# Performance work log

Hardware: AMD Instinct MI355X
Metric: run time of the kernel (lower is better)

The kernel has to match this reference:

```python
import jax, jax.numpy as jnp
import numpy as np

SG_SLOPE = 20.0  # fast_sigmoid surrogate slope
THRESHOLD = 1.0

@jax.custom_vjp
def spike_fn(v):
    # Heaviside spike with fast-sigmoid surrogate gradient
    return (v > 0).astype(v.dtype)

def _spike_fwd(v):
    return spike_fn(v), v

def _spike_bwd(v, g):
    return (g / (SG_SLOPE * jnp.abs(v) + 1.0) ** 2,)

spike_fn.defvjp(_spike_fwd, _spike_bwd)

def setup_inputs() -> dict:
    key = jax.random.key(0)
    T, IN, H, HEADS, O = 8192, 192, 1024, 5, 2
    dt = 0.004
    sp = float(np.log1p(np.exp(0.5413)))  # softplus(param) ~= 1.0
    tau_syn_h, tau_mem_h = 0.01 * sp, 0.02 * sp
    tau_syn_r = np.array([0.01, 0.02, 0.05, 0.1, 0.2]) * sp
    tau_mem_r = np.array([0.02, 0.05, 0.1, 0.2, 0.5]) * sp
    k1, k2, k3, k4 = jax.random.split(key, 4)
    x = jax.random.normal(k1, (T, IN), jnp.float32)
    W_in = jax.random.normal(k2, (H, IN), jnp.float32) / np.sqrt(IN)
    V = jax.random.normal(k3, (H, H), jnp.float32) / np.sqrt(H)
    b_rec = jnp.zeros((H,), jnp.float32)
    W_out = jax.random.normal(k4, (HEADS, O, H), jnp.float32) / np.sqrt(H)
    return {
        "x": x, "W_in": W_in, "V": V, "b_rec": b_rec, "W_out": W_out,
        "alpha_h": jnp.float32(np.exp(-dt / tau_syn_h)),
        "beta_h": jnp.float32(np.exp(-dt / tau_mem_h)),
        "alpha_r": jnp.asarray(np.exp(-dt / tau_syn_r), jnp.float32),
        "beta_r": jnp.asarray(np.exp(-dt / tau_mem_r), jnp.float32),
    }

def reference(x, W_in, V, b_rec, W_out, alpha_h, beta_h, alpha_r, beta_r):
    H = W_in.shape[0]
    HEADS, O, _ = W_out.shape
    dt_f32 = x.dtype

    def step(carry, x_t):
        inp_prev, spk, syn_h, mem_h, syn_r, mem_r = carry
        # hidden RSynaptic (note: fc_hidden consumes the PREVIOUS input, one-step delay)
        cur = W_in @ inp_prev + V @ spk + b_rec
        syn_h_new = alpha_h * syn_h + cur
        reset = jax.lax.stop_gradient(spk)  # zero-reset uses previous spike, detached
        mem_h_new = (beta_h * mem_h + syn_h_new) * (1.0 - reset)
        spk_new = spike_fn(mem_h_new - THRESHOLD)
        # readout heads consume the PREVIOUS hidden spike (pre-update)
        r_in = jnp.einsum("hoc,c->ho", W_out, spk)  # [HEADS, 2]
        syn_r_new = alpha_r[:, None] * syn_r + r_in
        mem_r_new = beta_r[:, None] * mem_r + syn_r_new  # reset_mechanism='none'
        out = mem_r_new.mean(axis=0)  # average over readout heads
        return (x_t, spk_new, syn_h_new, mem_h_new, syn_r_new, mem_r_new), out

    init = (
        jnp.zeros_like(x[0]),
        jnp.zeros((H,), dt_f32),
        jnp.zeros((H,), dt_f32),
        jnp.zeros((H,), dt_f32),
        jnp.zeros((HEADS, O), dt_f32),
        jnp.zeros((HEADS, O), dt_f32),
    )
    _, preds = jax.lax.scan(step, init, x)
    return preds  # [T, 2]
```

## Files before the change

kernel.cpp:

```cpp
#include <hip/hip_runtime.h>
#include <hip/hip_bf16.h>


constexpr int T_STEPS = 8192;
constexpr int IN_DIM  = 192;
constexpr int H_DIM   = 1024;
constexpr int NBLK    = 32;
constexpr int RING    = 4;

__global__ void k_clear(unsigned int* __restrict__ p, int n) {
    int i = blockIdx.x * blockDim.x + threadIdx.x;
    if (i < n) p[i] = 0u;
}

__global__ __launch_bounds__(576, 1) void k_phase1(
    const float* __restrict__ x,
    const float* __restrict__ W_in,
    const float* __restrict__ V,
    const float* __restrict__ b_rec,
    const float* __restrict__ alpha_h_p,
    const float* __restrict__ beta_h_p,
    unsigned long long* __restrict__ mbox,
    uint2* __restrict__ raster)
{
    const int tid   = threadIdx.x;
    const int blk   = blockIdx.x;
    const int w     = tid >> 6;
    const int l     = tid & 63;
    const bool syncw = (w == 8);
    const int r_local = l >> 4;
    const int cg      = l & 15;
    const int row   = (blk << 5) + (w << 2) + r_local;

    __shared__ unsigned int       bits_lds[RING][NBLK];
    __shared__ unsigned long long combine[2];
    __shared__ unsigned long long rdyPack;

    for (int i = tid; i < RING * NBLK; i += 576)
        ((unsigned int*)bits_lds)[i] = 0u;
    if (tid == 0) { combine[0] = 0ull; combine[1] = 0ull; rdyPack = 0ull; }

    unsigned int* rp = (unsigned int*)&rdyPack;

    float4 vfrag[16];
    float  wfrag[12];
    float  b_r = 0.f;
    if (!syncw) {
        const float4* vp = (const float4*)(V + (size_t)row * H_DIM + cg * 64);
        #pragma unroll
        for (int i = 0; i < 16; ++i) vfrag[i] = vp[i];
        const float* wp = W_in + row * IN_DIM + cg * 12;
        #pragma unroll
        for (int i = 0; i < 12; ++i) wfrag[i] = wp[i];
        b_r = b_rec[row];
    }
    const float ah = alpha_h_p[0];
    const float bh = beta_h_p[0];

    __syncthreads();

    float u0 = 1.02f, u1 = 1.03f, u2 = 1.05f, u3 = 1.07f;
    const float bc = 1.0000001f, bd = 1e-30f;

    if (syncw) {
        const bool act = (l < NBLK) && (l != blk);
        for (int t = 0; t < T_STEPS - 1; ++t) {
            const unsigned int want = (unsigned int)(t + 1);
            const unsigned long long* p =
                &mbox[(size_t)(((t & (RING - 1)) * NBLK + blk) * NBLK) + (l & 31)];
            unsigned long long vv = act
                ? __hip_atomic_load(p, __ATOMIC_RELAXED, __HIP_MEMORY_SCOPE_AGENT)
                : (((unsigned long long)want << 16) | ((unsigned long long)want << 48));
            bool ok = (((vv >> 16) & 0xffffull) == want) && ((vv >> 48) == want);
            while (__any(!ok)) {
                if (!ok)
                    vv = __hip_atomic_load(p, __ATOMIC_RELAXED,
                                           __HIP_MEMORY_SCOPE_AGENT);
                #pragma unroll
                for (int i = 0; i < 8; ++i) {
                    u0 = fmaf(u0, bc, bd); u1 = fmaf(u1, bc, bd);
                    u2 = fmaf(u2, bc, bd); u3 = fmaf(u3, bc, bd);
                }
                ok = (((vv >> 16) & 0xffffull) == want) && ((vv >> 48) == want);
            }
            if (act)
                bits_lds[t & (RING - 1)][l] =
                    (unsigned int)(vv & 0xffffull)
                    | ((unsigned int)((vv >> 32) & 0xffffull) << 16);
            asm volatile("s_waitcnt lgkmcnt(0)" ::: "memory");
            __builtin_amdgcn_sched_barrier(0);
            if (l == 0)
                __hip_atomic_store(&rp[0], (unsigned int)(t + 1),
                                   __ATOMIC_RELAXED, __HIP_MEMORY_SCOPE_WORKGROUP);
        }
    } else {
        const float* xptr = x + cg * 12;
        float xr[12];
        #pragma unroll
        for (int i = 0; i < 12; ++i) xr[i] = 0.0f;
        float syn = 0.f, mem = 0.f, prev = 0.f;

        for (int t = 0; t < T_STEPS; ++t) {
            const float4* xp4 = (const float4*)xptr;
            float4 f0 = xp4[0], f1 = xp4[1], f2 = xp4[2];

            unsigned long long rv = __hip_atomic_load(&rdyPack, __ATOMIC_ACQUIRE,
                                        __HIP_MEMORY_SCOPE_WORKGROUP);
            while ((unsigned int)rv < (unsigned int)t ||
                   (unsigned int)(rv >> 32) < (unsigned int)t) {
                #pragma unroll
                for (int i = 0; i < 4; ++i) {
                    u0 = fmaf(u0, bc, bd); u1 = fmaf(u1, bc, bd);
                    u2 = fmaf(u2, bc, bd); u3 = fmaf(u3, bc, bd);
                }
                rv = __hip_atomic_load(&rdyPack, __ATOMIC_ACQUIRE,
                                       __HIP_MEMORY_SCOPE_WORKGROUP);
            }

            const int slot = (t + RING - 1) & (RING - 1);
            unsigned int b0 = bits_lds[slot][2 * cg];
            unsigned int b1 = bits_lds[slot][2 * cg + 1];

            float a0 = 0.f, a1 = 0.f;
            #pragma unroll
            for (int i = 0; i < 8; ++i) {
                a0 = fmaf((float)((b0 >> (4 * i + 0)) & 1u), vfrag[i].x, a0);
                a0 = fmaf((float)((b0 >> (4 * i + 1)) & 1u), vfrag[i].y, a0);
                a0 = fmaf((float)((b0 >> (4 * i + 2)) & 1u), vfrag[i].z, a0);
                a0 = fmaf((float)((b0 >> (4 * i + 3)) & 1u), vfrag[i].w, a0);
                a1 = fmaf((float)((b1 >> (4 * i + 0)) & 1u), vfrag[8 + i].x, a1);
                a1 = fmaf((float)((b1 >> (4 * i + 1)) & 1u), vfrag[8 + i].y, a1);
                a1 = fmaf((float)((b1 >> (4 * i + 2)) & 1u), vfrag[8 + i].z, a1);
                a1 = fmaf((float)((b1 >> (4 * i + 3)) & 1u), vfrag[8 + i].w, a1);
            }
            #pragma unroll
            for (int i = 0; i < 12; ++i) a0 = fmaf(wfrag[i], xr[i], a0);
            float acc = a0 + a1;

            #pragma unroll
            for (int m = 1; m < 16; m <<= 1) acc += __shfl_xor(acc, m, 64);

            float cur = acc + b_r;
            syn = fmaf(ah, syn, cur);
            mem = fmaf(bh, mem, syn) * (1.0f - prev);
            float spk = (mem > 1.0f) ? 1.0f : 0.0f;
            prev = spk;

            unsigned long long bal = __ballot(spk > 0.5f);
            unsigned int isLast = 0u, bitsAll = 0u;
            if (l == 0) {
                unsigned int nib = (unsigned int)(bal & 1ull)
                                 | ((unsigned int)((bal >> 16) & 1ull) << 1)
                                 | ((unsigned int)((bal >> 32) & 1ull) << 2)
                                 | ((unsigned int)((bal >> 48) & 1ull) << 3);
                unsigned long long add =
                    (1ull << 32) | ((unsigned long long)nib << (4 * w));
                unsigned long long old = __hip_atomic_fetch_add(&combine[t & 1],
                        add, __ATOMIC_RELAXED, __HIP_MEMORY_SCOPE_WORKGROUP);
                unsigned long long nv = old + add;
                if ((nv >> 32) == 8ull) { isLast = 1u; bitsAll = (unsigned int)nv; }
            }
            isLast = __shfl(isLast, 0, 64);
            if (isLast) {
                unsigned int bits = __shfl(bitsAll, 0, 64);
                unsigned int want = (unsigned int)(t + 1);
                unsigned int w0t = (want << 16) | (bits & 0xffffu);
                unsigned int w1t = (want << 16) | (bits >> 16);
                unsigned long long pack =
                    (unsigned long long)w0t | ((unsigned long long)w1t << 32);
                if (l < NBLK && l != blk) {
                    __hip_atomic_store(
                        &mbox[(size_t)(((t & (RING - 1)) * NBLK + l) * NBLK) + blk],
                        pack, __ATOMIC_RELAXED, __HIP_MEMORY_SCOPE_AGENT);
                }
                if (l == 0) {
                    bits_lds[t & (RING - 1)][blk] = bits;
                    combine[t & 1] = 0ull;
                    asm volatile("s_waitcnt lgkmcnt(0)" ::: "memory");
                    __builtin_amdgcn_sched_barrier(0);
                    __hip_atomic_store(&rp[1], (unsigned int)(t + 1),
                                       __ATOMIC_RELAXED,
                                       __HIP_MEMORY_SCOPE_WORKGROUP);
                    raster[(size_t)t * NBLK + blk] = make_uint2(w0t, w1t);
                }
            }

            #pragma unroll
            for (int i = 0; i < 4; ++i) {
                xr[i]     = (&f0.x)[i];
                xr[4 + i] = (&f1.x)[i];
                xr[8 + i] = (&f2.x)[i];
            }
            xptr += IN_DIM;
        }
    }
    asm volatile("" :: "v"(u0), "v"(u1), "v"(u2), "v"(u3));
}

__global__ __launch_bounds__(256, 1) void k_readout_mm(
    const uint2* __restrict__ raster,
    const float* __restrict__ W_out,
    float* __restrict__ R)
{
    __shared__ float wlds[10 * 1033];
    for (int i = threadIdx.x; i < 10 * 1024; i += 256) {
        int r = i >> 10, c = i & 1023;
        wlds[r * 1033 + c] = W_out[i];
    }
    __syncthreads();

    int tid = threadIdx.x;
    if (tid >= 250) return;
    int tl = tid / 10, rowr = tid - tl * 10;
    int t = blockIdx.x * 25 + tl;
    if (t >= T_STEPS) return;

    float acc = 0.f;
    if (t > 0) {
        const uint2* wp = raster + (size_t)(t - 1) * NBLK;
        const float* wr = &wlds[rowr * 1033];
        for (int ww = 0; ww < NBLK; ++ww) {
            uint2 v = wp[ww];
            unsigned int bits = (v.x & 0xffffu) | ((v.y & 0xffffu) << 16);
            const float* wb = wr + ww * 32;
            #pragma unroll
            for (int j = 0; j < 32; ++j)
                acc = fmaf((float)((bits >> j) & 1u), wb[j], acc);
        }
    }
    R[t * 10 + rowr] = acc;
}

__global__ void k_scan(const float* __restrict__ R,
                       const float* __restrict__ alpha_r,
                       const float* __restrict__ beta_r,
                       float* __restrict__ memr_all)
{
    int lane = threadIdx.x;
    bool act = lane < 10;
    float a = act ? alpha_r[lane >> 1] : 0.f;
    float b = act ? beta_r[lane >> 1] : 0.f;
    float syn = 0.f, mem = 0.f;
    constexpr int PF = 8;
    float buf[PF];
    #pragma unroll
    for (int i = 0; i < PF; ++i) buf[i] = act ? R[i * 10 + lane] : 0.f;

    for (int tb = 0; tb < T_STEPS; tb += PF) {
        #pragma unroll
        for (int i = 0; i < PF; ++i) {
            int t = tb + i;
            syn = fmaf(a, syn, buf[i]);
            mem = fmaf(b, mem, syn);
            if (act) memr_all[t * 10 + lane] = mem;
            int tn = t + PF;
            buf[i] = (act && tn < T_STEPS) ? R[tn * 10 + lane] : 0.f;
        }
    }
}

__global__ void k_mean(const float* __restrict__ memr_all, float* __restrict__ out) {
    int g = blockIdx.x * blockDim.x + threadIdx.x;
    if (g >= T_STEPS * 2) return;
    int t = g >> 1, o = g & 1;
    const float* m = memr_all + t * 10 + o;
    out[g] = 0.2f * (m[0] + m[2] + m[4] + m[6] + m[8]);
}

extern "C" void kernel_launch(void* const* d_in, const int* in_sizes, int n_in,
                              void* d_out, int out_size, void* d_ws, size_t ws_size,
                              hipStream_t stream) {
    (void)in_sizes; (void)n_in; (void)out_size; (void)ws_size;
    const float* x       = (const float*)d_in[0];
    const float* W_in    = (const float*)d_in[1];
    const float* V       = (const float*)d_in[2];
    const float* b_rec   = (const float*)d_in[3];
    const float* W_out   = (const float*)d_in[4];
    const float* alpha_h = (const float*)d_in[5];
    const float* beta_h  = (const float*)d_in[6];
    const float* alpha_r = (const float*)d_in[7];
    const float* beta_r  = (const float*)d_in[8];
    float* out = (float*)d_out;

    char* wsb = (char*)d_ws;
    unsigned long long* mbox = (unsigned long long*)wsb;
    uint2* raster  = (uint2*)(wsb + RING * NBLK * NBLK * 8);
    float* Rbuf    = (float*)(wsb + RING * NBLK * NBLK * 8
                              + (size_t)T_STEPS * NBLK * 8);
    float* memr_all = Rbuf + (size_t)T_STEPS * 10;

    int nclr = RING * NBLK * NBLK * 2;
    k_clear<<<(nclr + 255) / 256, 256, 0, stream>>>((unsigned int*)mbox, nclr);
    k_phase1<<<NBLK, 576, 0, stream>>>(x, W_in, V, b_rec, alpha_h, beta_h,
                                       mbox, raster);
    k_readout_mm<<<(T_STEPS + 24) / 25, 256, 0, stream>>>(raster, W_out, Rbuf);
    k_scan<<<1, 64, 0, stream>>>(Rbuf, alpha_r, beta_r, memr_all);
    k_mean<<<(T_STEPS * 2 + 255) / 256, 256, 0, stream>>>(memr_all, out);
}
```

Measured before the change: 17.64 ms.

## Halve persistent workgroup count to 16 with 64 rows per block

Repartitions the recurrent step across 16 workgroups instead of 32, so each block owns 64 hidden rows and each lane holds twice as much of V in registers. The goal is fewer cross-block mailbox exchanges and pollers per timestep, cutting the global synchronisation latency that dominates the serial 8192-step loop. The intra-block spike combine is reworked around a 64-bit bit mask plus a separate counter, and the raster format becomes 64 bits per block. In exchange each lane does twice the FMA work and uses many more registers, and x is now loaded directly each step instead of being prefetched a step ahead.

Result: slower. 42.27 ms (+139.6%).

```diff
diff --git a/kernel.cpp b/kernel.cpp
--- a/kernel.cpp
+++ b/kernel.cpp
@@ -5,7 +5,7 @@
 constexpr int T_STEPS = 8192;
 constexpr int IN_DIM  = 192;
 constexpr int H_DIM   = 1024;
-constexpr int NBLK    = 32;
+constexpr int NBLK    = 16;
 constexpr int RING    = 4;
 
 __global__ void k_clear(unsigned int* __restrict__ p, int n) {
@@ -21,37 +21,44 @@
     const float* __restrict__ alpha_h_p,
     const float* __restrict__ beta_h_p,
     unsigned long long* __restrict__ mbox,
-    uint2* __restrict__ raster)
+    unsigned long long* __restrict__ raster)
 {
     const int tid   = threadIdx.x;
     const int blk   = blockIdx.x;
     const int w     = tid >> 6;
     const int l     = tid & 63;
     const bool syncw = (w == 8);
-    const int r_local = l >> 4;
-    const int cg      = l & 15;
-    const int row   = (blk << 5) + (w << 2) + r_local;
-
-    __shared__ unsigned int       bits_lds[RING][NBLK];
-    __shared__ unsigned long long combine[2];
+    const int r_local = l >> 3;
+    const int cg      = l & 7;
+    const int row   = (blk << 6) + (w << 3) + r_local;
+
+    __shared__ __align__(16) unsigned int bits_lds[RING][2 * NBLK];
+    __shared__ unsigned long long cbits[2];
+    __shared__ unsigned int       ccnt[2];
     __shared__ unsigned long long rdyPack;
 
-    for (int i = tid; i < RING * NBLK; i += 576)
+    for (int i = tid; i < RING * 2 * NBLK; i += 576)
         ((unsigned int*)bits_lds)[i] = 0u;
-    if (tid == 0) { combine[0] = 0ull; combine[1] = 0ull; rdyPack = 0ull; }
-
+    if (tid == 0) {
+        cbits[0] = 0ull; cbits[1] = 0ull;
+        ccnt[0] = 0u; ccnt[1] = 0u; rdyPack = 0ull;
+    }
     unsigned int* rp = (unsigned int*)&rdyPack;
 
-    float4 vfrag[16];
-    float  wfrag[12];
+    float4 vfrag[32];
+    float  wfrag[24];
     float  b_r = 0.f;
     if (!syncw) {
-        const float4* vp = (const float4*)(V + (size_t)row * H_DIM + cg * 64);
+        const float4* vp = (const float4*)(V + (size_t)row * H_DIM + cg * 128);
         #pragma unroll
-        for (int i = 0; i < 16; ++i) vfrag[i] = vp[i];
-        const float* wp = W_in + row * IN_DIM + cg * 12;
+        for (int i = 0; i < 32; ++i) vfrag[i] = vp[i];
+        const float4* wp = (const float4*)(W_in + row * IN_DIM + cg * 24);
         #pragma unroll
-        for (int i = 0; i < 12; ++i) wfrag[i] = wp[i];
+        for (int i = 0; i < 6; ++i) {
+            float4 v4 = wp[i];
+            wfrag[4 * i]     = v4.x; wfrag[4 * i + 1] = v4.y;
+            wfrag[4 * i + 2] = v4.z; wfrag[4 * i + 3] = v4.w;
+        }
         b_r = b_rec[row];
     }
     const float ah = alpha_h_p[0];
@@ -63,11 +70,12 @@
     const float bc = 1.0000001f, bd = 1e-30f;
 
     if (syncw) {
-        const bool act = (l < NBLK) && (l != blk);
+        const int p_idx = l >> 1;
+        const bool act = (l < 2 * NBLK) && (p_idx != blk);
         for (int t = 0; t < T_STEPS - 1; ++t) {
             const unsigned int want = (unsigned int)(t + 1);
             const unsigned long long* p =
-                &mbox[(size_t)(((t & (RING - 1)) * NBLK + blk) * NBLK) + (l & 31)];
+                &mbox[(size_t)(((t & (RING - 1)) * NBLK + blk) * 2 * NBLK) + (l & 31)];
             unsigned long long vv = act
                 ? __hip_atomic_load(p, __ATOMIC_RELAXED, __HIP_MEMORY_SCOPE_AGENT)
                 : (((unsigned long long)want << 16) | ((unsigned long long)want << 48));
@@ -84,7 +92,7 @@
                 ok = (((vv >> 16) & 0xffffull) == want) && ((vv >> 48) == want);
             }
             if (act)
-                bits_lds[t & (RING - 1)][l] =
+                bits_lds[t & (RING - 1)][l & 31] =
                     (unsigned int)(vv & 0xffffull)
                     | ((unsigned int)((vv >> 32) & 0xffffull) << 16);
             asm volatile("s_waitcnt lgkmcnt(0)" ::: "memory");
@@ -94,15 +102,19 @@
                                    __ATOMIC_RELAXED, __HIP_MEMORY_SCOPE_WORKGROUP);
         }
     } else {
-        const float* xptr = x + cg * 12;
-        float xr[12];
-        #pragma unroll
-        for (int i = 0; i < 12; ++i) xr[i] = 0.0f;
         float syn = 0.f, mem = 0.f, prev = 0.f;
 
         for (int t = 0; t < T_STEPS; ++t) {
-            const float4* xp4 = (const float4*)xptr;
-            float4 f0 = xp4[0], f1 = xp4[1], f2 = xp4[2];
+            float4 xf[6];
+            if (t > 0) {
+                const float4* xp4 =
+                    (const float4*)(x + (size_t)(t - 1) * IN_DIM + cg * 24);
+                #pragma unroll
+                for (int i = 0; i < 6; ++i) xf[i] = xp4[i];
+            } else {
+                #pragma unroll
+                for (int i = 0; i < 6; ++i) xf[i] = make_float4(0.f, 0.f, 0.f, 0.f);
+            }
 
             unsigned long long rv = __hip_atomic_load(&rdyPack, __ATOMIC_ACQUIRE,
                                         __HIP_MEMORY_SCOPE_WORKGROUP);
@@ -118,10 +130,10 @@
             }
 
             const int slot = (t + RING - 1) & (RING - 1);
-            unsigned int b0 = bits_lds[slot][2 * cg];
-            unsigned int b1 = bits_lds[slot][2 * cg + 1];
-
-            float a0 = 0.f, a1 = 0.f;
+            const uint4 bb = *reinterpret_cast<const uint4*>(&bits_lds[slot][4 * cg]);
+            const unsigned int b0 = bb.x, b1 = bb.y, b2 = bb.z, b3 = bb.w;
+
+            float a0 = 0.f, a1 = 0.f, a2 = 0.f, a3 = 0.f;
             #pragma unroll
             for (int i = 0; i < 8; ++i) {
                 a0 = fmaf((float)((b0 >> (4 * i + 0)) & 1u), vfrag[i].x, a0);
@@ -132,13 +144,26 @@
                 a1 = fmaf((float)((b1 >> (4 * i + 1)) & 1u), vfrag[8 + i].y, a1);
                 a1 = fmaf((float)((b1 >> (4 * i + 2)) & 1u), vfrag[8 + i].z, a1);
                 a1 = fmaf((float)((b1 >> (4 * i + 3)) & 1u), vfrag[8 + i].w, a1);
+                a2 = fmaf((float)((b2 >> (4 * i + 0)) & 1u), vfrag[16 + i].x, a2);
+                a2 = fmaf((float)((b2 >> (4 * i + 1)) & 1u), vfrag[16 + i].y, a2);
+                a2 = fmaf((float)((b2 >> (4 * i + 2)) & 1u), vfrag[16 + i].z, a2);
+                a2 = fmaf((float)((b2 >> (4 * i + 3)) & 1u), vfrag[16 + i].w, a2);
+                a3 = fmaf((float)((b3 >> (4 * i + 0)) & 1u), vfrag[24 + i].x, a3);
+                a3 = fmaf((float)((b3 >> (4 * i + 1)) & 1u), vfrag[24 + i].y, a3);
+                a3 = fmaf((float)((b3 >> (4 * i + 2)) & 1u), vfrag[24 + i].z, a3);
+                a3 = fmaf((float)((b3 >> (4 * i + 3)) & 1u), vfrag[24 + i].w, a3);
             }
             #pragma unroll
-            for (int i = 0; i < 12; ++i) a0 = fmaf(wfrag[i], xr[i], a0);
-            float acc = a0 + a1;
+            for (int i = 0; i < 6; ++i) {
+                a0 = fmaf(wfrag[4 * i],     xf[i].x, a0);
+                a1 = fmaf(wfrag[4 * i + 1], xf[i].y, a1);
+                a2 = fmaf(wfrag[4 * i + 2], xf[i].z, a2);
+                a3 = fmaf(wfrag[4 * i + 3], xf[i].w, a3);
+            }
+            float acc = (a0 + a1) + (a2 + a3);
 
             #pragma unroll
-            for (int m = 1; m < 16; m <<= 1) acc += __shfl_xor(acc, m, 64);
+            for (int m = 1; m < 8; m <<= 1) acc += __shfl_xor(acc, m, 64);
 
             float cur = acc + b_r;
             syn = fmaf(ah, syn, cur);
@@ -146,59 +171,67 @@
             float spk = (mem > 1.0f) ? 1.0f : 0.0f;
             prev = spk;
 
+            const int wsl = t & 1;
             unsigned long long bal = __ballot(spk > 0.5f);
-            unsigned int isLast = 0u, bitsAll = 0u;
+            unsigned int isLast = 0u;
+            unsigned long long bits64 = 0ull;
             if (l == 0) {
-                unsigned int nib = (unsigned int)(bal & 1ull)
-                                 | ((unsigned int)((bal >> 16) & 1ull) << 1)
-                                 | ((unsigned int)((bal >> 32) & 1ull) << 2)
-                                 | ((unsigned int)((bal >> 48) & 1ull) << 3);
-                unsigned long long add =
-                    (1ull << 32) | ((unsigned long long)nib << (4 * w));
-                unsigned long long old = __hip_atomic_fetch_add(&combine[t & 1],
-                        add, __ATOMIC_RELAXED, __HIP_MEMORY_SCOPE_WORKGROUP);
-                unsigned long long nv = old + add;
-                if ((nv >> 32) == 8ull) { isLast = 1u; bitsAll = (unsigned int)nv; }
+                unsigned int byte = 0u;
+                #pragma unroll
+                for (int r = 0; r < 8; ++r)
+                    byte |= ((unsigned int)(bal >> (8 * r)) & 1u) << r;
+                __hip_atomic_fetch_add(&cbits[wsl],
+                        (unsigned long long)byte << (8 * w),
+                        __ATOMIC_RELAXED, __HIP_MEMORY_SCOPE_WORKGROUP);
+                asm volatile("s_waitcnt lgkmcnt(0)" ::: "memory");
+                unsigned int oldc = __hip_atomic_fetch_add(&ccnt[wsl], 1u,
+                        __ATOMIC_RELAXED, __HIP_MEMORY_SCOPE_WORKGROUP);
+                if (oldc == 7u) {
+                    isLast = 1u;
+                    bits64 = __hip_atomic_load(&cbits[wsl], __ATOMIC_RELAXED,
+                                               __HIP_MEMORY_SCOPE_WORKGROUP);
+                }
             }
             isLast = __shfl(isLast, 0, 64);
             if (isLast) {
-                unsigned int bits = __shfl(bitsAll, 0, 64);
-                unsigned int want = (unsigned int)(t + 1);
-                unsigned int w0t = (want << 16) | (bits & 0xffffu);
-                unsigned int w1t = (want << 16) | (bits >> 16);
-                unsigned long long pack =
-                    (unsigned long long)w0t | ((unsigned long long)w1t << 32);
-                if (l < NBLK && l != blk) {
-                    __hip_atomic_store(
-                        &mbox[(size_t)(((t & (RING - 1)) * NBLK + l) * NBLK) + blk],
-                        pack, __ATOMIC_RELAXED, __HIP_MEMORY_SCOPE_AGENT);
+                bits64 = __shfl(bits64, 0, 64);
+                const unsigned int want = (unsigned int)(t + 1);
+                if (l < 2 * NBLK) {
+                    const int c = l >> 1, h = l & 1;
+                    if (c != blk) {
+                        unsigned int chunk = (unsigned int)(bits64 >> (32 * h));
+                        unsigned int w0t = (want << 16) | (chunk & 0xffffu);
+                        unsigned int w1t = (want << 16) | (chunk >> 16);
+                        unsigned long long pack =
+                            (unsigned long long)w0t | ((unsigned long long)w1t << 32);
+                        __hip_atomic_store(
+                            &mbox[(size_t)(((t & (RING - 1)) * NBLK + c) * 2 * NBLK)
+                                  + (blk * 2 + h)],
+                            pack, __ATOMIC_RELAXED, __HIP_MEMORY_SCOPE_AGENT);
+                    }
                 }
                 if (l == 0) {
-                    bits_lds[t & (RING - 1)][blk] = bits;
-                    combine[t & 1] = 0ull;
+                    bits_lds[t & (RING - 1)][blk * 2]     = (unsigned int)bits64;
+                    bits_lds[t & (RING - 1)][blk * 2 + 1] = (unsigned int)(bits64 >> 32);
+                    __hip_atomic_store(&cbits[wsl], 0ull, __ATOMIC_RELAXED,
+                                       __HIP_MEMORY_SCOPE_WORKGROUP);
+                    __hip_atomic_store(&ccnt[wsl], 0u, __ATOMIC_RELAXED,
+                                       __HIP_MEMORY_SCOPE_WORKGROUP);
                     asm volatile("s_waitcnt lgkmcnt(0)" ::: "memory");
                     __builtin_amdgcn_sched_barrier(0);
                     __hip_atomic_store(&rp[1], (unsigned int)(t + 1),
                                        __ATOMIC_RELAXED,
                                        __HIP_MEMORY_SCOPE_WORKGROUP);
-                    raster[(size_t)t * NBLK + blk] = make_uint2(w0t, w1t);
-                }
-            }
-
-            #pragma unroll
-            for (int i = 0; i < 4; ++i) {
-                xr[i]     = (&f0.x)[i];
-                xr[4 + i] = (&f1.x)[i];
-                xr[8 + i] = (&f2.x)[i];
-            }
-            xptr += IN_DIM;
+                    raster[(size_t)t * NBLK + blk] = bits64;
+                }
+            }
         }
     }
     asm volatile("" :: "v"(u0), "v"(u1), "v"(u2), "v"(u3));
 }
 
 __global__ __launch_bounds__(256, 1) void k_readout_mm(
-    const uint2* __restrict__ raster,
+    const unsigned long long* __restrict__ raster,
     const float* __restrict__ W_out,
     float* __restrict__ R)
 {
@@ -217,15 +250,14 @@
 
     float acc = 0.f;
     if (t > 0) {
-        const uint2* wp = raster + (size_t)(t - 1) * NBLK;
+        const unsigned long long* wp = raster + (size_t)(t - 1) * NBLK;
         const float* wr = &wlds[rowr * 1033];
         for (int ww = 0; ww < NBLK; ++ww) {
-            uint2 v = wp[ww];
-            unsigned int bits = (v.x & 0xffffu) | ((v.y & 0xffffu) << 16);
-            const float* wb = wr + ww * 32;
+            unsigned long long bits = wp[ww];
+            const float* wb = wr + ww * 64;
             #pragma unroll
-            for (int j = 0; j < 32; ++j)
-                acc = fmaf((float)((bits >> j) & 1u), wb[j], acc);
+            for (int j = 0; j < 64; ++j)
+                acc = fmaf((float)((bits >> j) & 1ull), wb[j], acc);
         }
     }
     R[t * 10 + rowr] = acc;
@@ -284,12 +316,13 @@
 
     char* wsb = (char*)d_ws;
     unsigned long long* mbox = (unsigned long long*)wsb;
-    uint2* raster  = (uint2*)(wsb + RING * NBLK * NBLK * 8);
-    float* Rbuf    = (float*)(wsb + RING * NBLK * NBLK * 8
+    unsigned long long* raster =
+        (unsigned long long*)(wsb + RING * NBLK * 2 * NBLK * 8);
+    float* Rbuf    = (float*)(wsb + RING * NBLK * 2 * NBLK * 8
                               + (size_t)T_STEPS * NBLK * 8);
     float* memr_all = Rbuf + (size_t)T_STEPS * 10;
 
-    int nclr = RING * NBLK * NBLK * 2;
+    int nclr = RING * NBLK * 2 * NBLK * 2;
     k_clear<<<(nclr + 255) / 256, 256, 0, stream>>>((unsigned int*)mbox, nclr);
     k_phase1<<<NBLK, 576, 0, stream>>>(x, W_in, V, b_rec, alpha_h, beta_h,
                                        mbox, raster);
```
